# Kernel tuning notes

Measured on AMD Instinct MI355X. Metric: run time of the kernel, lower is better.

Reference implementation:

```python
import jax, jax.numpy as jnp
import numpy as np

D, H, G, HD = 2048, 16, 4, 128  # d_model, num_heads, num_groups, head_dim
B, S = 2, 2048


def _rope(x):
    # x: [B, heads, S, HD]; RoPE with concat(freqs, freqs) layout (rotate_half style)
    seq = x.shape[2]
    inv_freq = 1.0 / (10000.0 ** (jnp.arange(0, HD, 2, dtype=jnp.float32) / HD))  # [HD/2]
    t = jnp.arange(seq, dtype=jnp.float32)
    freqs = t[:, None] * inv_freq[None, :]              # [S, HD/2]
    emb = jnp.concatenate([freqs, freqs], axis=-1)      # [S, HD]
    cos = jnp.cos(emb)[None, None]                      # [1,1,S,HD]
    sin = jnp.sin(emb)[None, None]
    x1, x2 = jnp.split(x, 2, axis=-1)
    rot = jnp.concatenate([-x2, x1], axis=-1)           # rotate_half
    return x * cos + rot * sin


def setup_inputs() -> dict:
    key = jax.random.key(0)
    ks = jax.random.split(key, 5)
    x = jax.random.normal(ks[0], (B, S, D), dtype=jnp.float32)
    # weights stored as [in, out] so y = x @ W (equivalent to torch Linear with W^T)
    Wq = jax.random.normal(ks[1], (D, D), dtype=jnp.float32) * 0.02
    Wk = jax.random.normal(ks[2], (D, G * HD), dtype=jnp.float32) * 0.02
    Wv = jax.random.normal(ks[3], (D, G * HD), dtype=jnp.float32) * 0.02
    Wo = jax.random.normal(ks[4], (D, D), dtype=jnp.float32) * 0.02
    # causal mask: True = masked (matches torch masked_fill semantics)
    mask = ~jnp.tril(jnp.ones((S, S), dtype=bool))[None, None]  # [1,1,S,S]
    return {"x": x, "Wq": Wq, "Wk": Wk, "Wv": Wv, "Wo": Wo, "mask": mask}


def reference(x, Wq, Wk, Wv, Wo, mask):
    b, s, _ = x.shape
    q = (x @ Wq).reshape(b, s, H, HD).transpose(0, 2, 1, 3)   # [B,H,S,HD]
    k = (x @ Wk).reshape(b, s, G, HD).transpose(0, 2, 1, 3)   # [B,G,S,HD]
    v = (x @ Wv).reshape(b, s, G, HD).transpose(0, 2, 1, 3)   # [B,G,S,HD]
    q = _rope(q)
    k = _rope(k)
    # GQA: repeat_interleave KV groups across heads
    k = jnp.repeat(k, H // G, axis=1)                         # [B,H,S,HD]
    v = jnp.repeat(v, H // G, axis=1)
    scale = jnp.float32(1.0 / np.sqrt(HD))
    scores = jnp.einsum('bhqd,bhkd->bhqk', q, k) * scale      # [B,H,S,S]
    scores = jnp.where(mask, jnp.float32(-1e9), scores)
    attn = jax.nn.softmax(scores, axis=-1)
    ctx = jnp.einsum('bhqk,bhkd->bhqd', attn, v)              # [B,H,S,HD]
    ctx = ctx.transpose(0, 2, 1, 3).reshape(b, s, D)
    return ctx @ Wo
```

## Files before the change

### kernel.cpp

```cpp
#include <hip/hip_runtime.h>
#include <hip/hip_bf16.h>
#include <math.h>

#define BB 2
#define SS 2048
#define DD 2048
#define HH 16
#define GG 4
#define HDIM 128
#define DKV (GG * HDIM)
#define MS (BB * SS)
#define QKVS 3072

typedef __attribute__((ext_vector_type(8))) short bf16x8;
typedef __attribute__((ext_vector_type(4))) float f32x4;
typedef __attribute__((ext_vector_type(4))) unsigned int u32x4;

#if __has_builtin(__builtin_amdgcn_exp2f)
#define EXP2F __builtin_amdgcn_exp2f
#else
#define EXP2F exp2f
#endif

__device__ __forceinline__ ushort f2bf(float x) {
    __hip_bfloat16 b = __float2bfloat16(x);
    return *(ushort*)&b;
}
__device__ __forceinline__ float bf2f(ushort u) {
    __hip_bfloat16 b;
    *(ushort*)&b = u;
    return __bfloat162float(b);
}

#define GLOAD_LDS(src, dst)                                                        \
    __builtin_amdgcn_global_load_lds(                                              \
        (const __attribute__((address_space(1))) unsigned int*)(src),              \
        (__attribute__((address_space(3))) unsigned int*)(dst), 16, 0, 0)

#define WAITV(n) asm volatile("s_waitcnt vmcnt(" #n ")" ::: "memory")

__global__ __launch_bounds__(256) void prep4(const float* __restrict__ x,
                                             const float* __restrict__ Wq,
                                             const float* __restrict__ Wk,
                                             const float* __restrict__ Wv,
                                             const float* __restrict__ Wo,
                                             ushort* __restrict__ xh,
                                             ushort* __restrict__ WqkvT,
                                             ushort* __restrict__ WoT) {
    __shared__ ushort tile[32][33];
    const int z = blockIdx.z;
    if (z == 4) {
        int idx = (blockIdx.y * 64 + blockIdx.x) * 256 + threadIdx.x;
        const float4* p = (const float4*)x + (size_t)idx * 2;
        float4 a = p[0], b = p[1];
        float v[8] = {a.x, a.y, a.z, a.w, b.x, b.y, b.z, b.w};
        ushort r[8];
#pragma unroll
        for (int j = 0; j < 8; ++j) r[j] = f2bf(v[j]);
        *((u32x4*)xh + idx) = *(u32x4*)r;
        return;
    }
    if ((z == 1 || z == 2) && blockIdx.x >= DKV / 32) return;
    const float* W = (z == 0) ? Wq : (z == 1) ? Wk : (z == 2) ? Wv : Wo;
    ushort* WT = (z == 3) ? WoT
                          : WqkvT + ((z == 0) ? (size_t)0
                                              : (z == 1) ? (size_t)DD * DD
                                                         : (size_t)(DD + DKV) * DD);
    const int N = (z == 1 || z == 2) ? DKV : DD;
    const int tx = threadIdx.x & 31, ty = threadIdx.x >> 5;
    const int n0 = blockIdx.x * 32, k0 = blockIdx.y * 32;
#pragma unroll
    for (int i = 0; i < 4; ++i)
        tile[ty + i * 8][tx] = f2bf(W[(size_t)(k0 + ty + i * 8) * N + n0 + tx]);
    __syncthreads();
#pragma unroll
    for (int i = 0; i < 4; ++i)
        WT[(size_t)(n0 + ty + i * 8) * DD + k0 + tx] = tile[tx][ty + i * 8];
}

__global__ __launch_bounds__(256) void rope_tv(ushort* __restrict__ QKV,
                                               ushort* __restrict__ VT) {
    __shared__ ushort tile[32][33];
    const int id = blockIdx.x;
    if (id < 2560) {
        int idx = id * 256 + threadIdx.x;
        int oct = idx & 7;
        int hh = (idx >> 3) % 20;
        int row = idx / (8 * 20);
        int s = row & (SS - 1);
        int colOff = (hh < 16) ? hh * HDIM : 2048 + (hh - 16) * HDIM;
        size_t base = (size_t)row * QKVS + colOff + oct * 8;
        u32x4 lo = *(u32x4*)&QKV[base];
        u32x4 hi = *(u32x4*)&QKV[base + 64];
        ushort* lp = (ushort*)&lo;
        ushort* hp = (ushort*)&hi;
        ushort ro[8], rh[8];
#pragma unroll
        for (int j = 0; j < 8; ++j) {
            int i = oct * 8 + j;
            float inv = exp2f((float)i * -0.2076205059304601f);
            float ang = (float)s * inv;
            float c, sn;
            __sincosf(ang, &sn, &c);
            float x1 = bf2f(lp[j]), x2 = bf2f(hp[j]);
            ro[j] = f2bf(x1 * c - x2 * sn);
            rh[j] = f2bf(x2 * c + x1 * sn);
        }
        *(u32x4*)&QKV[base] = *(u32x4*)ro;
        *(u32x4*)&QKV[base + 64] = *(u32x4*)rh;
        return;
    }
    const int lid = id - 2560;
    const int tx = threadIdx.x & 31, ty = threadIdx.x >> 5;
    const int d0 = (lid & 15) * 32;
    const int k0 = ((lid >> 4) & 63) * 32;
    const int b = lid >> 10;
#pragma unroll
    for (int i = 0; i < 4; ++i)
        tile[ty + i * 8][tx] =
            QKV[(size_t)(b * SS + k0 + ty + i * 8) * QKVS + 2560 + d0 + tx];
    __syncthreads();
    const int posl = ((tx & 12) << 1) | ((tx & 16) >> 2) | (tx & 3);
#pragma unroll
    for (int i = 0; i < 4; ++i)
        VT[((size_t)b * DKV + d0 + ty + i * 8) * SS + k0 + posl] = tile[tx][ty + i * 8];
}

template <int BN, bool OUT_BF16>
__global__ __launch_bounds__(512) void gemm8(const ushort* __restrict__ A,
                                             const ushort* __restrict__ BT,
                                             void* __restrict__ Cout,
                                             int M, int N, int K) {
    constexpr int ABUF = 128 * 32;
    constexpr int BBUF = BN * 32;
    constexpr int NWC = BN / 64;
    constexpr int NWM = 8 / NWC;
    constexpr int ROWS = 128 / NWM;
    constexpr int MFR = ROWS / 16;
    __shared__ ushort As[3 * ABUF];
    __shared__ ushort Bs[3 * BBUF];

    const int t = threadIdx.x;
    const int w = t >> 6, l = t & 63;
    const int lm = l & 15, lw = l >> 4;
    const int wr = w / NWC, wc = w % NWC;
    const int nx = gridDim.x;
    const int bid = blockIdx.y * nx + blockIdx.x;
    const int cpx = (nx * gridDim.y) >> 3;
    const int swb = (bid & 7) * cpx + (bid >> 3);
    const int bm = (swb / nx) * 128, bn = (swb % nx) * BN;

    const int NT = K >> 5;
    const int swzc = (lw ^ ((lm >> 1) & 3)) * 8;

    const int ar0 = t >> 2, ac0 = (t & 3) ^ ((ar0 >> 1) & 3);
    const ushort* a0 = A + (size_t)(bm + ar0) * K + ac0 * 8;
    const int br0 = t >> 2, bc0 = (t & 3) ^ ((br0 >> 1) & 3);
    const ushort* b0 = BT + (size_t)(bn + br0) * K + bc0 * 8;
    const int br1 = (t + 512) >> 2, bc1 = ((t + 512) & 3) ^ ((br1 >> 1) & 3);
    const ushort* b1 = BT + (size_t)(bn + br1) * K + bc1 * 8;

    auto STAGE = [&](int slot) {
        GLOAD_LDS(a0, &As[slot * ABUF + t * 8]);
        a0 += 32;
        GLOAD_LDS(b0, &Bs[slot * BBUF + t * 8]);
        b0 += 32;
        if constexpr (BN == 256) {
            GLOAD_LDS(b1, &Bs[slot * BBUF + (t + 512) * 8]);
            b1 += 32;
        }
    };

    f32x4 acc[MFR][4];
#pragma unroll
    for (int m = 0; m < MFR; ++m)
#pragma unroll
        for (int n = 0; n < 4; ++n) acc[m][n] = (f32x4){0.f, 0.f, 0.f, 0.f};

    STAGE(0);
    STAGE(1);
    int cs = 0, ps = 2;

#pragma unroll 1
    for (int kt = 0; kt < NT; ++kt) {
        if (kt + 1 < NT) {
            if constexpr (BN == 256) WAITV(3); else WAITV(2);
        } else {
            WAITV(0);
        }
        __builtin_amdgcn_s_barrier();
        if (kt + 2 < NT) STAGE(ps);

        const ushort* Ab = &As[cs * ABUF];
        const ushort* Bb = &Bs[cs * BBUF];
        bf16x8 bfr[4], af[MFR];
#pragma unroll
        for (int n = 0; n < 4; ++n)
            bfr[n] = *(const bf16x8*)&Bb[(wc * 64 + n * 16 + lm) * 32 + swzc];
#pragma unroll
        for (int i = 0; i < MFR; ++i)
            af[i] = *(const bf16x8*)&Ab[(wr * ROWS + i * 16 + lm) * 32 + swzc];
        __builtin_amdgcn_s_setprio(1);
#pragma unroll
        for (int i = 0; i < MFR; ++i)
#pragma unroll
            for (int n = 0; n < 4; ++n)
                acc[i][n] = __builtin_amdgcn_mfma_f32_16x16x32_bf16(af[i], bfr[n], acc[i][n], 0, 0, 0);
        __builtin_amdgcn_s_setprio(0);

        cs = (cs == 2) ? 0 : cs + 1;
        ps = (ps == 2) ? 0 : ps + 1;
    }

#pragma unroll
    for (int m = 0; m < MFR; ++m)
#pragma unroll
        for (int n = 0; n < 4; ++n)
#pragma unroll
            for (int r = 0; r < 4; ++r) {
                int row = bm + wr * ROWS + m * 16 + lw * 4 + r;
                int col = bn + wc * 64 + n * 16 + lm;
                if (OUT_BF16)
                    ((ushort*)Cout)[(size_t)row * N + col] = f2bf(acc[m][n][r]);
                else
                    ((float*)Cout)[(size_t)row * N + col] = acc[m][n][r];
            }
}

template <bool OUT_BF16>
__global__ __launch_bounds__(512) void gemm64(const ushort* __restrict__ A,
                                              const ushort* __restrict__ BT,
                                              void* __restrict__ Cout,
                                              int M, int N, int K) {
    __shared__ ushort As[2][128 * 64];
    __shared__ ushort Bs[2][128 * 64];
    const int t = threadIdx.x;
    const int w = t >> 6, l = t & 63;
    const int lm = l & 15, lw = l >> 4;
    const int wr = w >> 1, wc = w & 1;
    const int nx = gridDim.x;
    const int bid = blockIdx.y * nx + blockIdx.x;
    const int cpx = (nx * gridDim.y) >> 3;
    const int swb = (bid & 7) * cpx + (bid >> 3);
    const int bm = (swb / nx) * 128, bn = (swb % nx) * 128;
    const int NT = K >> 6;

    const int rowc = t >> 3, cc = t & 7;
    const int xb = (cc ^ (rowc & 7)) * 8;
    const ushort* a0 = A + (size_t)(bm + rowc) * K + xb;
    const ushort* a1 = A + (size_t)(bm + rowc + 64) * K + xb;
    const ushort* b0 = BT + (size_t)(bn + rowc) * K + xb;
    const ushort* b1 = BT + (size_t)(bn + rowc + 64) * K + xb;
    const int d0 = t * 8, d1 = (t + 512) * 8;

    auto STAGE = [&](int s) {
        GLOAD_LDS(a0, &As[s][d0]);
        a0 += 64;
        GLOAD_LDS(a1, &As[s][d1]);
        a1 += 64;
        GLOAD_LDS(b0, &Bs[s][d0]);
        b0 += 64;
        GLOAD_LDS(b1, &Bs[s][d1]);
        b1 += 64;
    };

    f32x4 acc[2][4];
#pragma unroll
    for (int m = 0; m < 2; ++m)
#pragma unroll
        for (int n = 0; n < 4; ++n) acc[m][n] = (f32x4){0.f, 0.f, 0.f, 0.f};

    STAGE(0);
    WAITV(0);
    __builtin_amdgcn_s_barrier();

    int buf = 0;
#pragma unroll 1
    for (int kt = 0; kt < NT; ++kt) {
        const bool more = (kt + 1 < NT);
        if (more) STAGE(buf ^ 1);

        bf16x8 af[2][2], bfr[4][2];
#pragma unroll
        for (int ks = 0; ks < 2; ++ks) {
            const int col = (((ks << 2) | lw) ^ (lm & 7)) * 8;
#pragma unroll
            for (int n = 0; n < 4; ++n)
                bfr[n][ks] = *(const bf16x8*)&Bs[buf][(wc * 64 + n * 16 + lm) * 64 + col];
#pragma unroll
            for (int i = 0; i < 2; ++i)
                af[i][ks] = *(const bf16x8*)&As[buf][(wr * 32 + i * 16 + lm) * 64 + col];
        }
        __builtin_amdgcn_s_setprio(1);
#pragma unroll
        for (int ks = 0; ks < 2; ++ks)
#pragma unroll
            for (int i = 0; i < 2; ++i)
#pragma unroll
                for (int n = 0; n < 4; ++n)
                    acc[i][n] = __builtin_amdgcn_mfma_f32_16x16x32_bf16(af[i][ks], bfr[n][ks], acc[i][n], 0, 0, 0);
        __builtin_amdgcn_s_setprio(0);

        if (more) {
            WAITV(0);
            __builtin_amdgcn_s_barrier();
        }
        buf ^= 1;
    }

#pragma unroll
    for (int m = 0; m < 2; ++m)
#pragma unroll
        for (int n = 0; n < 4; ++n)
#pragma unroll
            for (int r = 0; r < 4; ++r) {
                int row = bm + wr * 32 + m * 16 + lw * 4 + r;
                int col = bn + wc * 64 + n * 16 + lm;
                if (OUT_BF16)
                    ((ushort*)Cout)[(size_t)row * N + col] = f2bf(acc[m][n][r]);
                else
                    ((float*)Cout)[(size_t)row * N + col] = acc[m][n][r];
            }
}

#define SCL 0.08838834764831845f
#define CEXP 0.1275296340545927f
#define THRRAW 90.50966799187809f

__global__ __launch_bounds__(512) void attn_mfma(const ushort* __restrict__ QKV,
                                                 const ushort* __restrict__ VT,
                                                 ushort* __restrict__ Ctx) {
    __shared__ ushort Ks[2][128 * 128];
    __shared__ ushort Vs[2][128 * 128];
    const int t = threadIdx.x;
    const int w = t >> 6;
    const int l = t & 63;
    const int lm = l & 15, lw = l >> 4;
    const int bid = blockIdx.x;
    const int g = bid & 3;
    const int b = (bid >> 2) & 1;
    const int within = bid >> 3;
    const int xq = within & 7;
    const int h = g * 4 + (within >> 3);
    const int swz = (lm & 7) << 3;

    const ushort* kbase = QKV + (size_t)(b * SS) * QKVS + 2048 + g * HDIM;
    const ushort* vbase = VT + ((size_t)b * DKV + g * HDIM) * SS;

    const short one_bf = (short)0x3F80;
    const bf16x8 ones = {one_bf, one_bf, one_bf, one_bf, one_bf, one_bf, one_bf, one_bf};

    int krr[4], koo[4];
#pragma unroll
    for (int it = 0; it < 4; ++it) {
        int c = t + it * 512;
        krr[it] = c >> 4;
        koo[it] = (c & 15) ^ (krr[it] & 7);
    }

#pragma unroll 1
    for (int phase = 0; phase < 2; ++phase) {
        const int qt = (phase == 0) ? xq : (15 - xq);
        const int q0 = qt * 128;
        const int qw = q0 + w * 16;
        const int q = qw + lm;
        const int ntiles = qt + 1;

        const ushort* ks[4];
        const ushort* vs[4];
#pragma unroll
        for (int it = 0; it < 4; ++it) {
            ks[it] = kbase + (size_t)krr[it] * QKVS + koo[it] * 8;
            vs[it] = vbase + (size_t)krr[it] * SS + koo[it] * 8;
        }

        bf16x8 qa[4];
        {
            const ushort* qp = QKV + (size_t)(b * SS + qw + lm) * QKVS + h * HDIM + lw * 8;
#pragma unroll
            for (int kk = 0; kk < 4; ++kk)
                qa[kk] = *(const bf16x8*)(qp + kk * 32);
        }

        f32x4 acc[8];
#pragma unroll
        for (int d = 0; d < 8; ++d) acc[d] = (f32x4){0.f, 0.f, 0.f, 0.f};
        f32x4 accl = (f32x4){0.f, 0.f, 0.f, 0.f};
        float m = -INFINITY;

#pragma unroll
        for (int it = 0; it < 4; ++it) {
            GLOAD_LDS(ks[it], &Ks[0][(t + it * 512) * 8]);
            ks[it] += 128 * QKVS;
            GLOAD_LDS(vs[it], &Vs[0][(t + it * 512) * 8]);
            vs[it] += 128;
        }
        asm volatile("s_waitcnt vmcnt(0)" ::: "memory");
        __builtin_amdgcn_s_barrier();

#pragma unroll 1
        for (int tile = 0; tile < ntiles; ++tile) {
            const int cur = tile & 1;
            const int kv0 = tile * 128;
            const bool more = (tile + 1 < ntiles);
            if (more) {
                ushort* kd = &Ks[cur ^ 1][0];
                ushort* vd = &Vs[cur ^ 1][0];
#pragma unroll
                for (int it = 0; it < 4; ++it) {
                    GLOAD_LDS(ks[it], kd + (t + it * 512) * 8);
                    ks[it] += 128 * QKVS;
                    GLOAD_LDS(vs[it], vd + (t + it * 512) * 8);
                    vs[it] += 128;
                }
            }

            f32x4 sfT[8];
#pragma unroll
            for (int kvb = 0; kvb < 8; ++kvb) sfT[kvb] = (f32x4){0.f, 0.f, 0.f, 0.f};
            __builtin_amdgcn_s_setprio(1);
#pragma unroll
            for (int kvb = 0; kvb < 8; ++kvb)
#pragma unroll
                for (int kk = 0; kk < 4; ++kk) {
                    bf16x8 kb = *(const bf16x8*)&Ks[cur][(kvb * 16 + lm) * 128 + ((kk * 32 + lw * 8) ^ swz)];
                    sfT[kvb] = __builtin_amdgcn_mfma_f32_16x16x32_bf16(kb, qa[kk], sfT[kvb], 0, 0, 0);
                }
            __builtin_amdgcn_s_setprio(0);

            if (tile == ntiles - 1) {
#pragma unroll
                for (int kvb = 0; kvb < 8; ++kvb)
#pragma unroll
                    for (int r = 0; r < 4; ++r) {
                        int kv = kv0 + kvb * 16 + lw * 4 + r;
                        if (kv > q) sfT[kvb][r] = -INFINITY;
                    }
            }

            float rm = fmaxf(fmaxf(sfT[0][0], sfT[0][1]), fmaxf(sfT[0][2], sfT[0][3]));
#pragma unroll
            for (int kvb = 1; kvb < 8; ++kvb)
                rm = fmaxf(rm, fmaxf(fmaxf(sfT[kvb][0], sfT[kvb][1]),
                                     fmaxf(sfT[kvb][2], sfT[kvb][3])));
            rm = fmaxf(rm, __shfl_xor(rm, 16));
            rm = fmaxf(rm, __shfl_xor(rm, 32));

            bool stable = (rm - m <= THRRAW);
            if (!__all((int)stable)) {
                float mn = fmaxf(m, rm);
                float alpha_l = EXP2F((m - mn) * CEXP);
                m = mn;
                float ar[4];
#pragma unroll
                for (int r = 0; r < 4; ++r)
                    ar[r] = __shfl(alpha_l, (l & 48) | (lw * 4 + r));
#pragma unroll
                for (int d = 0; d < 8; ++d) {
                    acc[d][0] *= ar[0];
                    acc[d][1] *= ar[1];
                    acc[d][2] *= ar[2];
                    acc[d][3] *= ar[3];
                }
                accl[0] *= ar[0];
                accl[1] *= ar[1];
                accl[2] *= ar[2];
                accl[3] *= ar[3];
            }

            bf16x8 pa[4];
            float mC = m * CEXP;
#pragma unroll
            for (int kvb = 0; kvb < 8; ++kvb)
#pragma unroll
                for (int r = 0; r < 4; ++r) {
                    float pv = EXP2F(fmaf(sfT[kvb][r], CEXP, -mC));
                    pa[kvb >> 1][(kvb & 1) * 4 + r] = (short)f2bf(pv);
                }

            __builtin_amdgcn_s_setprio(1);
#pragma unroll
            for (int kks = 0; kks < 4; ++kks) {
                accl = __builtin_amdgcn_mfma_f32_16x16x32_bf16(pa[kks], ones, accl, 0, 0, 0);
#pragma unroll
                for (int dcol = 0; dcol < 8; ++dcol) {
                    bf16x8 vb = *(const bf16x8*)&Vs[cur][(dcol * 16 + lm) * 128 + ((kks * 32 + lw * 8) ^ swz)];
                    acc[dcol] = __builtin_amdgcn_mfma_f32_16x16x32_bf16(pa[kks], vb, acc[dcol], 0, 0, 0);
                }
            }
            __builtin_amdgcn_s_setprio(0);

            if (more) {
                asm volatile("s_waitcnt vmcnt(0)" ::: "memory");
                __builtin_amdgcn_s_barrier();
            }
        }

        float rinv[4];
#pragma unroll
        for (int r = 0; r < 4; ++r) rinv[r] = 1.f / accl[r];
        ushort* cp = Ctx + (size_t)(b * SS + qw) * DD + h * HDIM;
#pragma unroll
        for (int d = 0; d < 8; ++d)
#pragma unroll
            for (int r = 0; r < 4; ++r)
                cp[(size_t)(lw * 4 + r) * DD + d * 16 + lm] = f2bf(acc[d][r] * rinv[r]);
        __builtin_amdgcn_s_barrier();
    }
}

extern "C" void kernel_launch(void* const* d_in, const int* in_sizes, int n_in,
                              void* d_out, int out_size, void* d_ws, size_t ws_size,
                              hipStream_t stream) {
    const float* x  = (const float*)d_in[0];
    const float* Wq = (const float*)d_in[1];
    const float* Wk = (const float*)d_in[2];
    const float* Wv = (const float*)d_in[3];
    const float* Wo = (const float*)d_in[4];
    float* out = (float*)d_out;

    ushort* xh    = (ushort*)d_ws;
    ushort* QKV   = xh + (size_t)MS * DD;
    ushort* VTb   = QKV + (size_t)MS * QKVS;
    ushort* WqkvT = VTb + (size_t)MS * DKV;
    ushort* WoT   = WqkvT + (size_t)QKVS * DD;
    ushort* Ch    = xh;

    dim3 blk(256);

    prep4<<<dim3(DD / 32, DD / 32, 5), blk, 0, stream>>>(x, Wq, Wk, Wv, Wo, xh, WqkvT, WoT);

    gemm8<128, true><<<dim3(QKVS / 128, MS / 128), dim3(512), 0, stream>>>(xh, WqkvT, QKV, MS, QKVS, DD);

    rope_tv<<<dim3(2560 + 2048), blk, 0, stream>>>(QKV, VTb);

    attn_mfma<<<dim3(256), dim3(512), 0, stream>>>(QKV, VTb, Ch);

    gemm64<false><<<dim3(DD / 128, MS / 128), dim3(512), 0, stream>>>(Ch, WoT, out, MS, DD, DD);
}
```

Baseline: 186.0 us.

## Fuse RoPE into QKV GEMM epilogue and drop separate rope pass

The QKV projection GEMM now assigns each wave column fragments that pair dimension i with i+64 inside one head. This lets RoPE be applied in the epilogue on the fp32 accumulators before they are stored as bf16. The standalone kernel that re-read and re-wrote Q and K for RoPE is reduced to only the V transpose, which removes one read and one write pass over the Q/K data. The cost is extra sincos work inside the GEMM epilogue, plus a less contiguous column mapping for the B-fragment reads.

```diff
diff --git a/kernel.cpp b/kernel.cpp
--- a/kernel.cpp
+++ b/kernel.cpp
@@ -78,39 +78,10 @@
         WT[(size_t)(n0 + ty + i * 8) * DD + k0 + tx] = tile[tx][ty + i * 8];
 }
 
-__global__ __launch_bounds__(256) void rope_tv(ushort* __restrict__ QKV,
-                                               ushort* __restrict__ VT) {
+__global__ __launch_bounds__(256) void transpose_v(const ushort* __restrict__ QKV,
+                                                   ushort* __restrict__ VT) {
     __shared__ ushort tile[32][33];
-    const int id = blockIdx.x;
-    if (id < 2560) {
-        int idx = id * 256 + threadIdx.x;
-        int oct = idx & 7;
-        int hh = (idx >> 3) % 20;
-        int row = idx / (8 * 20);
-        int s = row & (SS - 1);
-        int colOff = (hh < 16) ? hh * HDIM : 2048 + (hh - 16) * HDIM;
-        size_t base = (size_t)row * QKVS + colOff + oct * 8;
-        u32x4 lo = *(u32x4*)&QKV[base];
-        u32x4 hi = *(u32x4*)&QKV[base + 64];
-        ushort* lp = (ushort*)&lo;
-        ushort* hp = (ushort*)&hi;
-        ushort ro[8], rh[8];
-#pragma unroll
-        for (int j = 0; j < 8; ++j) {
-            int i = oct * 8 + j;
-            float inv = exp2f((float)i * -0.2076205059304601f);
-            float ang = (float)s * inv;
-            float c, sn;
-            __sincosf(ang, &sn, &c);
-            float x1 = bf2f(lp[j]), x2 = bf2f(hp[j]);
-            ro[j] = f2bf(x1 * c - x2 * sn);
-            rh[j] = f2bf(x2 * c + x1 * sn);
-        }
-        *(u32x4*)&QKV[base] = *(u32x4*)ro;
-        *(u32x4*)&QKV[base + 64] = *(u32x4*)rh;
-        return;
-    }
-    const int lid = id - 2560;
+    const int lid = blockIdx.x;
     const int tx = threadIdx.x & 31, ty = threadIdx.x >> 5;
     const int d0 = (lid & 15) * 32;
     const int k0 = ((lid >> 4) & 63) * 32;
@@ -126,50 +97,42 @@
         VT[((size_t)b * DKV + d0 + ty + i * 8) * SS + k0 + posl] = tile[tx][ty + i * 8];
 }
 
-template <int BN, bool OUT_BF16>
-__global__ __launch_bounds__(512) void gemm8(const ushort* __restrict__ A,
-                                             const ushort* __restrict__ BT,
-                                             void* __restrict__ Cout,
-                                             int M, int N, int K) {
+__global__ __launch_bounds__(512) void gemm_qkv(const ushort* __restrict__ A,
+                                                const ushort* __restrict__ BT,
+                                                ushort* __restrict__ C,
+                                                int M, int N, int K) {
     constexpr int ABUF = 128 * 32;
-    constexpr int BBUF = BN * 32;
-    constexpr int NWC = BN / 64;
-    constexpr int NWM = 8 / NWC;
-    constexpr int ROWS = 128 / NWM;
-    constexpr int MFR = ROWS / 16;
+    constexpr int BBUF = 128 * 32;
+    constexpr int ROWS = 32;
+    constexpr int MFR = 2;
     __shared__ ushort As[3 * ABUF];
     __shared__ ushort Bs[3 * BBUF];
 
     const int t = threadIdx.x;
     const int w = t >> 6, l = t & 63;
     const int lm = l & 15, lw = l >> 4;
-    const int wr = w / NWC, wc = w % NWC;
+    const int wr = w >> 1, wc = w & 1;
     const int nx = gridDim.x;
     const int bid = blockIdx.y * nx + blockIdx.x;
     const int cpx = (nx * gridDim.y) >> 3;
     const int swb = (bid & 7) * cpx + (bid >> 3);
-    const int bm = (swb / nx) * 128, bn = (swb % nx) * BN;
+    const int bm = (swb / nx) * 128, bn = (swb % nx) * 128;
 
     const int NT = K >> 5;
     const int swzc = (lw ^ ((lm >> 1) & 3)) * 8;
 
     const int ar0 = t >> 2, ac0 = (t & 3) ^ ((ar0 >> 1) & 3);
     const ushort* a0 = A + (size_t)(bm + ar0) * K + ac0 * 8;
-    const int br0 = t >> 2, bc0 = (t & 3) ^ ((br0 >> 1) & 3);
-    const ushort* b0 = BT + (size_t)(bn + br0) * K + bc0 * 8;
-    const int br1 = (t + 512) >> 2, bc1 = ((t + 512) & 3) ^ ((br1 >> 1) & 3);
-    const ushort* b1 = BT + (size_t)(bn + br1) * K + bc1 * 8;
+    const ushort* b0 = BT + (size_t)(bn + ar0) * K + ac0 * 8;
 
     auto STAGE = [&](int slot) {
         GLOAD_LDS(a0, &As[slot * ABUF + t * 8]);
         a0 += 32;
         GLOAD_LDS(b0, &Bs[slot * BBUF + t * 8]);
         b0 += 32;
-        if constexpr (BN == 256) {
-            GLOAD_LDS(b1, &Bs[slot * BBUF + (t + 512) * 8]);
-            b1 += 32;
-        }
     };
+
+    const int ncol[4] = {wc * 32, wc * 32 + 16, wc * 32 + 64, wc * 32 + 80};
 
     f32x4 acc[MFR][4];
 #pragma unroll
@@ -184,7 +147,7 @@
 #pragma unroll 1
     for (int kt = 0; kt < NT; ++kt) {
         if (kt + 1 < NT) {
-            if constexpr (BN == 256) WAITV(3); else WAITV(2);
+            WAITV(2);
         } else {
             WAITV(0);
         }
@@ -196,7 +159,7 @@
         bf16x8 bfr[4], af[MFR];
 #pragma unroll
         for (int n = 0; n < 4; ++n)
-            bfr[n] = *(const bf16x8*)&Bb[(wc * 64 + n * 16 + lm) * 32 + swzc];
+            bfr[n] = *(const bf16x8*)&Bb[(ncol[n] + lm) * 32 + swzc];
 #pragma unroll
         for (int i = 0; i < MFR; ++i)
             af[i] = *(const bf16x8*)&Ab[(wr * ROWS + i * 16 + lm) * 32 + swzc];
@@ -212,19 +175,36 @@
         ps = (ps == 2) ? 0 : ps + 1;
     }
 
-#pragma unroll
-    for (int m = 0; m < MFR; ++m)
-#pragma unroll
-        for (int n = 0; n < 4; ++n)
-#pragma unroll
-            for (int r = 0; r < 4; ++r) {
-                int row = bm + wr * ROWS + m * 16 + lw * 4 + r;
-                int col = bn + wc * 64 + n * 16 + lm;
-                if (OUT_BF16)
-                    ((ushort*)Cout)[(size_t)row * N + col] = f2bf(acc[m][n][r]);
-                else
-                    ((float*)Cout)[(size_t)row * N + col] = acc[m][n][r];
-            }
+    if (bn < 2560) {
+#pragma unroll
+        for (int n = 0; n < 2; ++n) {
+            const int i = wc * 32 + n * 16 + lm;
+            const float inv = exp2f((float)i * -0.2076205059304601f);
+#pragma unroll
+            for (int m = 0; m < MFR; ++m)
+#pragma unroll
+                for (int r = 0; r < 4; ++r) {
+                    int row = bm + wr * ROWS + m * 16 + lw * 4 + r;
+                    float ang = (float)(row & (SS - 1)) * inv;
+                    float c, sn;
+                    __sincosf(ang, &sn, &c);
+                    float x1 = acc[m][n][r], x2 = acc[m][n + 2][r];
+                    size_t base = (size_t)row * QKVS + bn + ncol[n] + lm;
+                    C[base] = f2bf(x1 * c - x2 * sn);
+                    C[base + 64] = f2bf(x2 * c + x1 * sn);
+                }
+        }
+    } else {
+#pragma unroll
+        for (int m = 0; m < MFR; ++m)
+#pragma unroll
+            for (int n = 0; n < 4; ++n)
+#pragma unroll
+                for (int r = 0; r < 4; ++r) {
+                    int row = bm + wr * ROWS + m * 16 + lw * 4 + r;
+                    C[(size_t)row * QKVS + bn + ncol[n] + lm] = f2bf(acc[m][n][r]);
+                }
+    }
 }
 
 template <bool OUT_BF16>
@@ -530,9 +510,9 @@
 
     prep4<<<dim3(DD / 32, DD / 32, 5), blk, 0, stream>>>(x, Wq, Wk, Wv, Wo, xh, WqkvT, WoT);
 
-    gemm8<128, true><<<dim3(QKVS / 128, MS / 128), dim3(512), 0, stream>>>(xh, WqkvT, QKV, MS, QKVS, DD);
-
-    rope_tv<<<dim3(2560 + 2048), blk, 0, stream>>>(QKV, VTb);
+    gemm_qkv<<<dim3(QKVS / 128, MS / 128), dim3(512), 0, stream>>>(xh, WqkvT, QKV, MS, QKVS, DD);
+
+    transpose_v<<<dim3(2048), blk, 0, stream>>>(QKV, VTb);
 
     attn_mfma<<<dim3(256), dim3(512), 0, stream>>>(QKV, VTb, Ch);
 
```

Result: faster. 181.4 us (median of 2 runs) (-2.5%).
